# Performance work log

Measured on AMD Instinct MI355X. Metric: run time of the kernel, lower is better.

## Reference

```python
import jax, jax.numpy as jnp
import numpy as np

N, H, W = 128, 192, 192
THING = 81            # cfg.MODEL.SOGNET.THING_NUM_CLASSES
CLS_DIM = 128         # cls_embedding_dim
POS_DIM = 64          # pos_embedding_dim
REL_DIM = CLS_DIM + POS_DIM


def setup_inputs() -> dict:
    key = jax.random.key(0)
    ks = jax.random.split(key, 8)
    mask_logits = jax.random.normal(ks[0], (1, N, H, W), dtype=jnp.float32)
    # valid boxes: x_max > x_min, y_max > y_min (log(w/h) must be finite)
    xy = jax.random.uniform(ks[1], (N, 2), minval=0.0, maxval=800.0)
    wh = jax.random.uniform(ks[2], (N, 2), minval=16.0, maxval=256.0)
    bbox = jnp.concatenate([xy, xy + wh], axis=1).astype(jnp.float32)
    cls_idx = jax.random.randint(ks[3], (N,), 1, THING)  # values in [1, 80]
    # params (kaiming-normal-ish scale)
    W_U = jax.random.normal(ks[4], (THING - 1, CLS_DIM), jnp.float32) * (2.0 / (THING - 1)) ** 0.5
    W_V = jax.random.normal(ks[5], (THING - 1, CLS_DIM), jnp.float32) * (2.0 / (THING - 1)) ** 0.5
    W_pos = jax.random.normal(ks[6], (4, POS_DIM), jnp.float32) * (2.0 / 4.0) ** 0.5
    W_P = jax.random.normal(ks[7], (REL_DIM, 1), jnp.float32) * (2.0 / REL_DIM) ** 0.5
    return {"mask_logits": mask_logits, "bbox": bbox, "W_U": W_U, "W_V": W_V,
            "W_pos": W_pos, "W_P": W_P, "cls_idx": cls_idx}


def _position_matrix(bbox):
    x_min, y_min, x_max, y_max = bbox[:, 0], bbox[:, 1], bbox[:, 2], bbox[:, 3]
    w = x_max - x_min
    h = y_max - y_min
    x_ctr = (x_min + x_max) / 2.0
    y_ctr = (y_min + y_max) / 2.0
    dx = -(x_ctr[:, None] - x_ctr[None, :]) / w[:, None]          # [N, N]
    dy = -(y_ctr[:, None] - y_ctr[None, :]) / h[:, None]
    dw = jnp.log(w[None, :] / w[:, None])                          # log(w_j / w_i)
    dh = jnp.log(h[None, :] / h[:, None])
    return jnp.stack([dx, dy, dw, dh], axis=2)                     # [N, N, 4]


def reference(mask_logits, bbox, W_U, W_V, W_pos, W_P, cls_idx):
    # --- class relation: outer product of two relu'd class embeddings ---
    one_hot = jax.nn.one_hot(cls_idx - 1, THING - 1, dtype=mask_logits.dtype)  # [N, 80]
    feat1 = jax.nn.relu(one_hot @ W_U)                             # [N, CLS_DIM]
    feat2 = jax.nn.relu(one_hot @ W_V)
    cls_rel = feat1[:, None, :] * feat2[None, :, :]                # [N, N, CLS_DIM]
    # --- position relation: 1x1 conv == linear over last dim ---
    pos_rel = jax.nn.relu(jnp.einsum('ijk,kd->ijd', _position_matrix(bbox), W_pos))  # [N, N, POS_DIM]
    # --- relation score ---
    relation_feat = jnp.concatenate([cls_rel, pos_rel], axis=2)    # [N, N, REL_DIM]
    overlap_score = jax.nn.sigmoid(jnp.einsum('ijk,k->ij', relation_feat, W_P[:, 0]))  # [N, N]
    relation_score = jax.nn.relu(overlap_score - overlap_score.T)  # [N, N]
    # --- relation-weighted mask aggregation ---
    # naive: sum_m (ml*mp)[b,n] * mp[b,m] * score[n,m]  -> factor the m-reduction as a GEMM
    mask_prob = jax.nn.sigmoid(mask_logits)                        # [1, N, H, W]
    weighted = jnp.einsum('nm,bmhw->bnhw', relation_score, mask_prob)
    overlap_part = mask_logits * mask_prob * weighted              # [1, N, H, W]
    return mask_logits - overlap_part
```

## Files before the change

### kernel.cpp

```cpp
#include <hip/hip_runtime.h>

#define HW    36864
#define PX    144
#define RST   136

typedef unsigned short u16;
typedef unsigned int   u32;
typedef __attribute__((ext_vector_type(8))) short bf16x8;
typedef __attribute__((ext_vector_type(4))) float f32x4;

__device__ __forceinline__ float bf2f(u32 u) {
    union { u32 i; float f; } c; c.i = u << 16; return c.f;
}
__device__ __forceinline__ u16 f2bf(float f) {
    union { float f; u32 i; } c; c.f = f;
    u32 r = (c.i + 0x7fffu + ((c.i >> 16) & 1u)) >> 16;
    return (u16)r;
}
__device__ __forceinline__ u32 pack2(float a, float b) {
    return (u32)f2bf(a) | ((u32)f2bf(b) << 16);
}
__device__ __forceinline__ float sigf(float x) { return 1.0f / (1.0f + __expf(-x)); }

__device__ __forceinline__ void unpack8(uint4 v, float* o) {
    o[0] = bf2f(v.x & 0xffffu); o[1] = bf2f(v.x >> 16);
    o[2] = bf2f(v.y & 0xffffu); o[3] = bf2f(v.y >> 16);
    o[4] = bf2f(v.z & 0xffffu); o[5] = bf2f(v.z >> 16);
    o[6] = bf2f(v.w & 0xffffu); o[7] = bf2f(v.w >> 16);
}

template<int BF16>
__device__ __forceinline__ float ld1(const void* p, int idx) {
    return BF16 ? bf2f((u32)((const u16*)p)[idx]) : ((const float*)p)[idx];
}

template<int BF16>
__device__ __forceinline__ bool wrong_dtype(const void* ml, int tid) {
    int pred = 0;
    if (tid < 128) {
        u16 v = ((const u16*)ml)[tid];
        u32 e = (v >> 7) & 0xffu;
        pred = ((v & 0x7fffu) == 0 || (e >= 90u && e <= 140u)) ? 1 : 0;
    }
    int cnt = __syncthreads_count(pred);
    return (cnt >= 100) != (BF16 != 0);
}

template<int BF16>
__global__ __launch_bounds__(128) void k_rel(
    const void* __restrict__ ml,   const void* __restrict__ bbox,
    const void* __restrict__ WU,   const void* __restrict__ WV,
    const void* __restrict__ Wpos, const void* __restrict__ WP,
    const int* __restrict__ cls,   u16* __restrict__ relN)
{
    const int n = blockIdx.x, m = threadIdx.x;
    if (wrong_dtype<BF16>(ml, m)) return;

    __shared__ float u_s[128], v_s[128], wpos_s[256], wpp_s[64], bbn_s[4];

    const int cn = cls[n] - 1;
    {
        float wp = ld1<BF16>(WP, m);
        u_s[m] = fmaxf(ld1<BF16>(WU, cn * 128 + m), 0.f) * wp;
        v_s[m] = fmaxf(ld1<BF16>(WV, cn * 128 + m), 0.f) * wp;
    }
    wpos_s[m]       = ld1<BF16>(Wpos, m);
    wpos_s[128 + m] = ld1<BF16>(Wpos, 128 + m);
    if (m < 64) wpp_s[m] = ld1<BF16>(WP, 128 + m);
    if (m < 4)  bbn_s[m] = ld1<BF16>(bbox, n * 4 + m);
    __syncthreads();

    const int cm = cls[m] - 1;
    float s1 = 0.f, s2 = 0.f;
    #pragma unroll 8
    for (int c = 0; c < 128; ++c) {
        float wv = ld1<BF16>(WV, cm * 128 + c);
        float wu = ld1<BF16>(WU, cm * 128 + c);
        s1 += u_s[c] * fmaxf(wv, 0.f);
        s2 += v_s[c] * fmaxf(wu, 0.f);
    }

    const float xmn = bbn_s[0], ymn = bbn_s[1], xMn = bbn_s[2], yMn = bbn_s[3];
    const float wn = xMn - xmn, hn = yMn - ymn;
    const float xcn = 0.5f * (xmn + xMn), ycn = 0.5f * (ymn + yMn);
    const float xmm = ld1<BF16>(bbox, m * 4 + 0), ymm = ld1<BF16>(bbox, m * 4 + 1);
    const float xMm = ld1<BF16>(bbox, m * 4 + 2), yMm = ld1<BF16>(bbox, m * 4 + 3);
    const float wm = xMm - xmm, hm = yMm - ymm;
    const float xcm = 0.5f * (xmm + xMm), ycm = 0.5f * (ymm + yMm);

    const float p0 = -(xcn - xcm) / wn, p1 = -(ycn - ycm) / hn;
    const float p2 = __logf(wm / wn),   p3 = __logf(hm / hn);
    const float q0 = -(xcm - xcn) / wm, q1 = -(ycm - ycn) / hm;
    const float q2 = __logf(wn / wm),   q3 = __logf(hn / hm);

    #pragma unroll 8
    for (int d = 0; d < 64; ++d) {
        float w0 = wpos_s[d], w1 = wpos_s[64 + d], w2 = wpos_s[128 + d], w3 = wpos_s[192 + d];
        float wp = wpp_s[d];
        float t1 = p0 * w0 + p1 * w1 + p2 * w2 + p3 * w3;
        float t2 = q0 * w0 + q1 * w1 + q2 * w2 + q3 * w3;
        s1 += fmaxf(t1, 0.f) * wp;
        s2 += fmaxf(t2, 0.f) * wp;
    }

    float r = fmaxf(sigf(s1) - sigf(s2), 0.f);
    relN[n * 128 + m] = f2bf(r);
}

template<int BF16>
__global__ __launch_bounds__(256) void k_main(
    const void* __restrict__ mlv, const u16* __restrict__ relN,
    void* __restrict__ outv)
{
    const int tid = threadIdx.x;
    if (wrong_dtype<BF16>(mlv, tid)) return;

    __shared__ u16 rel_s[128 * RST];
    __shared__ u16 prob_s[64 * PX];

    const int px0 = blockIdx.x * PX;
    const int w    = tid >> 6;
    const int lane = tid & 63;
    const int col  = lane & 15;
    const int quad = lane >> 4;
    const int n0   = w * 32;

    for (int idx = tid; idx < 2048; idx += 256) {
        int r = idx >> 4, c = idx & 15;
        uint4 v = ((const uint4*)relN)[idx];
        *(uint4*)(rel_s + r * RST + c * 8) = v;
    }

    f32x4 acc[2][9];
    #pragma unroll
    for (int i = 0; i < 2; ++i)
        #pragma unroll
        for (int t = 0; t < 9; ++t) acc[i][t] = (f32x4){0.f, 0.f, 0.f, 0.f};

    for (int h = 0; h < 2; ++h) {
        __syncthreads();
        for (int idx = tid; idx < 1152; idx += 256) {
            int r = idx / 18, c = idx - r * 18;
            size_t base = (size_t)(h * 64 + r) * HW + px0 + c * 8;
            float f[8];
            if (BF16) {
                uint4 v = *(const uint4*)((const u16*)mlv + base);
                unpack8(v, f);
            } else {
                float4 v0 = *(const float4*)((const float*)mlv + base);
                float4 v1 = *(const float4*)((const float*)mlv + base + 4);
                f[0] = v0.x; f[1] = v0.y; f[2] = v0.z; f[3] = v0.w;
                f[4] = v1.x; f[5] = v1.y; f[6] = v1.z; f[7] = v1.w;
            }
            uint4 o;
            o.x = pack2(sigf(f[0]), sigf(f[1]));
            o.y = pack2(sigf(f[2]), sigf(f[3]));
            o.z = pack2(sigf(f[4]), sigf(f[5]));
            o.w = pack2(sigf(f[6]), sigf(f[7]));
            *(uint4*)(prob_s + r * PX + c * 8) = o;
        }
        __syncthreads();

        #pragma unroll
        for (int ksl = 0; ksl < 2; ++ksl) {
            const int k0 = h * 64 + ksl * 32 + quad * 8;
            bf16x8 a0 = *(const bf16x8*)(rel_s + (n0 + col) * RST + k0);
            bf16x8 a1 = *(const bf16x8*)(rel_s + (n0 + 16 + col) * RST + k0);
            const u16* bbase = prob_s + (ksl * 32 + quad * 8) * PX + col;
            #pragma unroll
            for (int t = 0; t < 9; ++t) {
                const u16* bp = bbase + t * 16;
                bf16x8 bfrag;
                #pragma unroll
                for (int j = 0; j < 8; ++j) bfrag[j] = (short)bp[j * PX];
                acc[0][t] = __builtin_amdgcn_mfma_f32_16x16x32_bf16(a0, bfrag, acc[0][t], 0, 0, 0);
                acc[1][t] = __builtin_amdgcn_mfma_f32_16x16x32_bf16(a1, bfrag, acc[1][t], 0, 0, 0);
            }
        }
    }

    #pragma unroll
    for (int i = 0; i < 2; ++i) {
        #pragma unroll
        for (int t = 0; t < 9; ++t) {
            const int nb = n0 + i * 16 + quad * 4;
            const int px = px0 + t * 16 + col;
            #pragma unroll
            for (int r = 0; r < 4; ++r) {
                size_t off = (size_t)(nb + r) * HW + px;
                float mlvv = BF16 ? bf2f((u32)((const u16*)mlv)[off])
                                  : ((const float*)mlv)[off];
                float pr = sigf(mlvv);
                float o  = mlvv - mlvv * pr * acc[i][t][r];
                if (BF16) ((u16*)outv)[off] = f2bf(o);
                else      ((float*)outv)[off] = o;
            }
        }
    }
}

extern "C" void kernel_launch(void* const* d_in, const int* in_sizes, int n_in,
                              void* d_out, int out_size, void* d_ws, size_t ws_size,
                              hipStream_t stream) {
    const void* ml   = d_in[0];
    const void* bbox = d_in[1];
    const void* WU   = d_in[2];
    const void* WV   = d_in[3];
    const void* Wpos = d_in[4];
    const void* WP   = d_in[5];
    const int*  cls  = (const int*)d_in[6];

    u16* relN = (u16*)d_ws;

    k_rel<1><<<dim3(128), dim3(128), 0, stream>>>(ml, bbox, WU, WV, Wpos, WP, cls, relN);
    k_rel<0><<<dim3(128), dim3(128), 0, stream>>>(ml, bbox, WU, WV, Wpos, WP, cls, relN);
    k_main<1><<<dim3(256), dim3(256), 0, stream>>>(ml, relN, d_out);
    k_main<0><<<dim3(256), dim3(256), 0, stream>>>(ml, relN, d_out);
}
```

Measured before the change: 105.8 us.

## Stage MFMA results in LDS and vectorize epilogue global loads/stores

The epilogue previously did scalar strided global reads and writes per accumulator element. Accumulators are now rounded to bf16 and written into shared memory, then re-read row-wise so each thread handles 8 contiguous pixels with vector loads and stores. The probability tile stride is padded and B-fragment packing is done with u32 ops to reduce LDS bank conflicts. The bf16 rounding of the weighted sum adds a little precision loss, and the extra barriers and LDS round trip add some overhead.

```diff
diff --git a/kernel.cpp b/kernel.cpp
--- a/kernel.cpp
+++ b/kernel.cpp
@@ -3,6 +3,8 @@
 #define HW    36864
 #define PX    144
 #define RST   136
+#define PSTR  150
+#define WSTR  152
 
 typedef unsigned short u16;
 typedef unsigned int   u32;
@@ -115,10 +117,11 @@
     const int tid = threadIdx.x;
     if (wrong_dtype<BF16>(mlv, tid)) return;
 
-    __shared__ u16 rel_s[128 * RST];
-    __shared__ u16 prob_s[64 * PX];
-
-    const int px0 = blockIdx.x * PX;
+    __shared__ u16 smem[27008];
+    u16* rel_s  = smem;
+    u16* prob_s = smem + 17408;
+
+    const int px0  = blockIdx.x * PX;
     const int w    = tid >> 6;
     const int lane = tid & 63;
     const int col  = lane & 15;
@@ -152,49 +155,81 @@
                 f[0] = v0.x; f[1] = v0.y; f[2] = v0.z; f[3] = v0.w;
                 f[4] = v1.x; f[5] = v1.y; f[6] = v1.z; f[7] = v1.w;
             }
-            uint4 o;
-            o.x = pack2(sigf(f[0]), sigf(f[1]));
-            o.y = pack2(sigf(f[2]), sigf(f[3]));
-            o.z = pack2(sigf(f[4]), sigf(f[5]));
-            o.w = pack2(sigf(f[6]), sigf(f[7]));
-            *(uint4*)(prob_s + r * PX + c * 8) = o;
+            u16* dst = prob_s + r * PSTR + c * 8;
+            *(u32*)(dst + 0) = pack2(sigf(f[0]), sigf(f[1]));
+            *(u32*)(dst + 2) = pack2(sigf(f[2]), sigf(f[3]));
+            *(u32*)(dst + 4) = pack2(sigf(f[4]), sigf(f[5]));
+            *(u32*)(dst + 6) = pack2(sigf(f[6]), sigf(f[7]));
         }
         __syncthreads();
 
         #pragma unroll
         for (int ksl = 0; ksl < 2; ++ksl) {
-            const int k0 = h * 64 + ksl * 32 + quad * 8;
-            bf16x8 a0 = *(const bf16x8*)(rel_s + (n0 + col) * RST + k0);
-            bf16x8 a1 = *(const bf16x8*)(rel_s + (n0 + 16 + col) * RST + k0);
-            const u16* bbase = prob_s + (ksl * 32 + quad * 8) * PX + col;
+            const int k0g = h * 64 + ksl * 32 + quad * 8;
+            bf16x8 a0 = *(const bf16x8*)(rel_s + (n0 + col) * RST + k0g);
+            bf16x8 a1 = *(const bf16x8*)(rel_s + (n0 + 16 + col) * RST + k0g);
+            const u16* bbase = prob_s + (ksl * 32 + quad * 8) * PSTR + col;
             #pragma unroll
             for (int t = 0; t < 9; ++t) {
-                const u16* bp = bbase + t * 16;
-                bf16x8 bfrag;
-                #pragma unroll
-                for (int j = 0; j < 8; ++j) bfrag[j] = (short)bp[j * PX];
-                acc[0][t] = __builtin_amdgcn_mfma_f32_16x16x32_bf16(a0, bfrag, acc[0][t], 0, 0, 0);
-                acc[1][t] = __builtin_amdgcn_mfma_f32_16x16x32_bf16(a1, bfrag, acc[1][t], 0, 0, 0);
+                const u16* q = bbase + t * 16;
+                u32 g0 = q[0 * PSTR], g1 = q[1 * PSTR], g2 = q[2 * PSTR], g3 = q[3 * PSTR];
+                u32 g4 = q[4 * PSTR], g5 = q[5 * PSTR], g6 = q[6 * PSTR], g7 = q[7 * PSTR];
+                union { bf16x8 v; u32 u[4]; } bu;
+                bu.u[0] = g0 | (g1 << 16);
+                bu.u[1] = g2 | (g3 << 16);
+                bu.u[2] = g4 | (g5 << 16);
+                bu.u[3] = g6 | (g7 << 16);
+                acc[0][t] = __builtin_amdgcn_mfma_f32_16x16x32_bf16(a0, bu.v, acc[0][t], 0, 0, 0);
+                acc[1][t] = __builtin_amdgcn_mfma_f32_16x16x32_bf16(a1, bu.v, acc[1][t], 0, 0, 0);
             }
         }
     }
 
+    __syncthreads();
+    u16* wgt = smem;
     #pragma unroll
-    for (int i = 0; i < 2; ++i) {
-        #pragma unroll
-        for (int t = 0; t < 9; ++t) {
-            const int nb = n0 + i * 16 + quad * 4;
-            const int px = px0 + t * 16 + col;
+    for (int i = 0; i < 2; ++i)
+        #pragma unroll
+        for (int t = 0; t < 9; ++t)
             #pragma unroll
-            for (int r = 0; r < 4; ++r) {
-                size_t off = (size_t)(nb + r) * HW + px;
-                float mlvv = BF16 ? bf2f((u32)((const u16*)mlv)[off])
-                                  : ((const float*)mlv)[off];
-                float pr = sigf(mlvv);
-                float o  = mlvv - mlvv * pr * acc[i][t][r];
-                if (BF16) ((u16*)outv)[off] = f2bf(o);
-                else      ((float*)outv)[off] = o;
-            }
+            for (int r = 0; r < 4; ++r)
+                wgt[(n0 + i * 16 + quad * 4 + r) * WSTR + t * 16 + col] = f2bf(acc[i][t][r]);
+    __syncthreads();
+
+    #pragma unroll
+    for (int s = 0; s < 9; ++s) {
+        int chunk = tid + 256 * s;
+        int n = chunk / 18, c = chunk - n * 18;
+        size_t off = (size_t)n * HW + px0 + c * 8;
+        float f[8];
+        if (BF16) {
+            uint4 v = *(const uint4*)((const u16*)mlv + off);
+            unpack8(v, f);
+        } else {
+            float4 v0 = *(const float4*)((const float*)mlv + off);
+            float4 v1 = *(const float4*)((const float*)mlv + off + 4);
+            f[0] = v0.x; f[1] = v0.y; f[2] = v0.z; f[3] = v0.w;
+            f[4] = v1.x; f[5] = v1.y; f[6] = v1.z; f[7] = v1.w;
+        }
+        uint4 wv = *(const uint4*)(wgt + n * WSTR + c * 8);
+        float wf[8]; unpack8(wv, wf);
+        float o[8];
+        #pragma unroll
+        for (int j = 0; j < 8; ++j) {
+            float pr = sigf(f[j]);
+            o[j] = f[j] - f[j] * pr * wf[j];
+        }
+        if (BF16) {
+            uint4 ov;
+            ov.x = pack2(o[0], o[1]); ov.y = pack2(o[2], o[3]);
+            ov.z = pack2(o[4], o[5]); ov.w = pack2(o[6], o[7]);
+            *(uint4*)((u16*)outv + off) = ov;
+        } else {
+            float4 a, b;
+            a.x = o[0]; a.y = o[1]; a.z = o[2]; a.w = o[3];
+            b.x = o[4]; b.y = o[5]; b.z = o[6]; b.w = o[7];
+            *(float4*)((float*)outv + off) = a;
+            *(float4*)((float*)outv + off + 4) = b;
         }
     }
 }
```

New measurement: 106.1 us. About the same (+0.2%).
